# Kernel tuning notes

Hardware: AMD Instinct MI355X
Metric: run time of the kernel (lower is better)

## Reference

```python
import jax, jax.numpy as jnp
import numpy as np

OUT = 7            # output_size
SR = 2             # sampling_ratio (samples per bin per axis)
SCALES = (0.25, 0.125, 0.0625, 0.03125)
CANON_SIZE = 224.0
CANON_LVL = 4.0
MIN_LVL = 2
IMG = 800.0


def setup_inputs() -> dict:
    key = jax.random.key(0)
    kf = jax.random.split(key, 6)
    B, C, R = 2, 256, 256
    sizes = [200, 100, 50, 25]
    feats = [jax.random.normal(kf[i], (B, C, s, s), jnp.float32) for i, s in enumerate(sizes)]
    # valid xyxy boxes in [0, IMG], log-uniform side lengths -> spread across FPN levels
    ctr = jax.random.uniform(kf[4], (B, R, 2), minval=0.0, maxval=IMG)
    wh = jnp.exp(jax.random.uniform(kf[5], (B, R, 2), minval=float(np.log(16.0)), maxval=float(np.log(512.0))))
    lo = jnp.clip(ctr - wh / 2, 0.0, IMG)
    hi = jnp.clip(ctr + wh / 2, 0.0, IMG)
    boxes = jnp.concatenate([lo, hi], axis=-1)  # [B,R,4]
    return {"feat0": feats[0], "feat1": feats[1], "feat2": feats[2], "feat3": feats[3], "boxes": boxes}


def _prep(c, lim):
    """torchvision ROIAlign (aligned=False) bilinear index prep.
    c: sample coords [N,OUT,SR]; lim: per-box feature extent (H or W) [N]."""
    limb = lim[:, None, None]
    valid = (c > -1.0) & (c < limb)          # out-of-range samples contribute 0
    cc = jnp.maximum(c, 0.0)
    low = jnp.floor(cc)
    cap = limb - 1.0
    at_edge = low >= cap                      # y_low >= H-1 -> clamp, frac = 0
    low = jnp.minimum(low, cap)
    high = jnp.minimum(low + 1.0, cap)
    cc = jnp.where(at_edge, low, cc)
    frac = cc - low
    return valid, low.astype(jnp.int32), high.astype(jnp.int32), frac


def roi_pooler(feats, boxes):
    B, R = boxes.shape[0], boxes.shape[1]
    C = feats[0].shape[1]
    N = B * R
    flat = boxes.reshape(N, 4)
    bidx = jnp.repeat(jnp.arange(B, dtype=jnp.int32), R)  # batch index per ROI

    # level assignment (assign_boxes_to_levels)
    area = (flat[:, 2] - flat[:, 0]) * (flat[:, 3] - flat[:, 1])
    lvl = jnp.floor(CANON_LVL + jnp.log2(jnp.sqrt(area) / CANON_SIZE + 1e-8))
    lvl = jnp.clip(lvl, MIN_LVL, MIN_LVL + len(feats) - 1).astype(jnp.int32) - MIN_LVL  # [N] in [0,3]

    # pad all levels to P2 size and stack so each ROI is sampled once at its level
    Hm, Wm = feats[0].shape[2], feats[0].shape[3]
    padded = jnp.stack([jnp.pad(f, ((0, 0), (0, 0), (0, Hm - f.shape[2]), (0, Wm - f.shape[3]))) for f in feats])
    fp = padded.transpose(0, 1, 3, 4, 2)  # [L,B,Hm,Wm,C] channels-last for gather
    Hs = jnp.array([f.shape[2] for f in feats], jnp.float32)[lvl]
    Ws = jnp.array([f.shape[3] for f in feats], jnp.float32)[lvl]
    scale = jnp.array(SCALES, jnp.float32)[lvl]

    # ROIAlign aligned=False: scale coords, clamp roi size to >= 1
    x1 = flat[:, 0] * scale
    y1 = flat[:, 1] * scale
    x2 = flat[:, 2] * scale
    y2 = flat[:, 3] * scale
    roi_w = jnp.maximum(x2 - x1, 1.0)
    roi_h = jnp.maximum(y2 - y1, 1.0)
    bw = roi_w / OUT
    bh = roi_h / OUT

    # sample grid: bin index + sub-sample offsets -> [N,OUT,SR]
    grid = jnp.arange(OUT, dtype=jnp.float32)[None, :, None] + (jnp.arange(SR, dtype=jnp.float32)[None, None, :] + 0.5) / SR
    ys = y1[:, None, None] + bh[:, None, None] * grid
    xs = x1[:, None, None] + bw[:, None, None] * grid

    vy, yl, yh, fy = _prep(ys, Hs)
    vx, xl, xh, fx = _prep(xs, Ws)

    P = OUT * OUT * SR * SR  # all sample points per ROI

    def by(a):  # y-axis quantity -> broadcast over (out_y,out_x,sr_y,sr_x)
        return jnp.broadcast_to(a[:, :, None, :, None], (N, OUT, OUT, SR, SR)).reshape(N, P)

    def bx(a):
        return jnp.broadcast_to(a[:, None, :, None, :], (N, OUT, OUT, SR, SR)).reshape(N, P)

    YL, YH, FY, VY = by(yl), by(yh), by(fy), by(vy)
    XL, XH, FX, VX = bx(xl), bx(xh), bx(fx), bx(vx)

    li = lvl[:, None]
    bi = bidx[:, None]
    v00 = fp[li, bi, YL, XL]  # [N,P,C]
    v01 = fp[li, bi, YL, XH]
    v10 = fp[li, bi, YH, XL]
    v11 = fp[li, bi, YH, XH]

    w = lambda a: a[..., None]
    val = (w((1 - FY) * (1 - FX)) * v00 + w((1 - FY) * FX) * v01
           + w(FY * (1 - FX)) * v10 + w(FY * FX) * v11)
    val = val * w((VY & VX).astype(val.dtype))
    out = val.reshape(N, OUT, OUT, SR * SR, C).mean(axis=3)  # average over SR*SR samples
    return out.transpose(0, 3, 1, 2)  # [N,C,OUT,OUT]


def reference(feat0, feat1, feat2, feat3, boxes):
    return roi_pooler([feat0, feat1, feat2, feat3], boxes)
```

## Files before the change

### kernel.cpp

```cpp
#include <hip/hip_runtime.h>
#include <math.h>

#define OUTSZ 7
#define SRATE 2

#define B_ 2
#define C_ 256
#define R_ 256

__global__ __launch_bounds__(256) void roi_pooler_kernel(
    const float* __restrict__ f0, const float* __restrict__ f1,
    const float* __restrict__ f2, const float* __restrict__ f3,
    const float* __restrict__ boxes, float* __restrict__ out)
{
    const int total = B_ * R_ * C_ * OUTSZ * OUTSZ;
    int idx = blockIdx.x * blockDim.x + threadIdx.x;
    if (idx >= total) return;

    int ox = idx % OUTSZ;
    int oy = (idx / OUTSZ) % OUTSZ;
    int c  = (idx / (OUTSZ * OUTSZ)) % C_;
    int n  = idx / (OUTSZ * OUTSZ * C_);
    int b  = n / R_;

    const float* bx = boxes + (size_t)n * 4;
    float x1 = bx[0], y1 = bx[1], x2 = bx[2], y2 = bx[3];
    float area = (x2 - x1) * (y2 - y1);
    float lf = floorf(4.0f + log2f(sqrtf(area) / 224.0f + 1e-8f));
    lf = fminf(fmaxf(lf, 2.0f), 5.0f);
    int lvl = (int)lf - 2;

    const float scales[4] = {0.25f, 0.125f, 0.0625f, 0.03125f};
    const int   sizes[4]  = {200, 100, 50, 25};
    float scale = scales[lvl];
    int   HW    = sizes[lvl];
    const float* fptr;
    switch (lvl) {
        case 0:  fptr = f0; break;
        case 1:  fptr = f1; break;
        case 2:  fptr = f2; break;
        default: fptr = f3; break;
    }

    float fx1 = x1 * scale, fy1 = y1 * scale;
    float fx2 = x2 * scale, fy2 = y2 * scale;
    float roi_w = fmaxf(fx2 - fx1, 1.0f);
    float roi_h = fmaxf(fy2 - fy1, 1.0f);
    float bw = roi_w / OUTSZ;
    float bh = roi_h / OUTSZ;

    const float* plane = fptr + ((size_t)b * C_ + c) * (size_t)(HW * HW);
    float lim = (float)HW;
    float cap = lim - 1.0f;

    float acc = 0.0f;
    #pragma unroll
    for (int sy = 0; sy < SRATE; sy++) {
        float yc = fy1 + bh * ((float)oy + ((float)sy + 0.5f) / SRATE);
        bool  vy  = (yc > -1.0f) && (yc < lim);
        float ccy = fmaxf(yc, 0.0f);
        float lowy = floorf(ccy);
        bool  ey  = lowy >= cap;
        lowy = fminf(lowy, cap);
        float highy = fminf(lowy + 1.0f, cap);
        float wfy = ey ? 0.0f : (ccy - lowy);
        int yl = (int)lowy, yh = (int)highy;

        #pragma unroll
        for (int sx = 0; sx < SRATE; sx++) {
            float xc = fx1 + bw * ((float)ox + ((float)sx + 0.5f) / SRATE);
            bool  vx  = (xc > -1.0f) && (xc < lim);
            float ccx = fmaxf(xc, 0.0f);
            float lowx = floorf(ccx);
            bool  ex  = lowx >= cap;
            lowx = fminf(lowx, cap);
            float highx = fminf(lowx + 1.0f, cap);
            float wfx = ex ? 0.0f : (ccx - lowx);
            int xl = (int)lowx, xh = (int)highx;

            if (vy && vx) {
                float v00 = plane[yl * HW + xl];
                float v01 = plane[yl * HW + xh];
                float v10 = plane[yh * HW + xl];
                float v11 = plane[yh * HW + xh];
                acc += (1.0f - wfy) * (1.0f - wfx) * v00
                     + (1.0f - wfy) * wfx          * v01
                     + wfy          * (1.0f - wfx) * v10
                     + wfy          * wfx          * v11;
            }
        }
    }

    out[idx] = acc * (1.0f / (SRATE * SRATE));
}

extern "C" void kernel_launch(void* const* d_in, const int* in_sizes, int n_in,
                              void* d_out, int out_size, void* d_ws, size_t ws_size,
                              hipStream_t stream) {
    const float* f0    = (const float*)d_in[0];
    const float* f1    = (const float*)d_in[1];
    const float* f2    = (const float*)d_in[2];
    const float* f3    = (const float*)d_in[3];
    const float* boxes = (const float*)d_in[4];
    float* out = (float*)d_out;

    const int total = B_ * R_ * C_ * OUTSZ * OUTSZ;
    int block = 256;
    int grid = (total + block - 1) / block;
    roi_pooler_kernel<<<grid, block, 0, stream>>>(f0, f1, f2, f3, boxes, out);
}
```

Before: 221.3 us.

## Precompute per-ROI sampling tables and stage ROI patches in shared memory

Adds a prep kernel that computes the level, patch bounds and per-axis bilinear indices and weights for each ROI once, writing them to workspace. The main kernel gives each block one ROI and four channels. It cooperatively loads the ROI's feature patch into LDS with row-contiguous reads, then computes the 49 bins per channel from LDS. Patches too large for LDS fall back to direct global reads. This removes redundant per-thread coordinate math and scattered gathers, at the cost of an extra launch, workspace use, and idle threads (60 of 256) during compute.

```diff
diff --git a/kernel.cpp b/kernel.cpp
--- a/kernel.cpp
+++ b/kernel.cpp
@@ -3,25 +3,24 @@
 
 #define OUTSZ 7
 #define SRATE 2
-
 #define B_ 2
 #define C_ 256
 #define R_ 256
+#define N_ (B_ * R_)
 
-__global__ __launch_bounds__(256) void roi_pooler_kernel(
-    const float* __restrict__ f0, const float* __restrict__ f1,
-    const float* __restrict__ f2, const float* __restrict__ f3,
-    const float* __restrict__ boxes, float* __restrict__ out)
+#define SPAD 1232
+
+struct RoiInfo {
+    int lvl, HW, planeBase0, x0, y0, Wp, Hp, S;
+    float wy0[14], wy1[14], wx0[14], wx1[14];
+    short ylr[14], yhr[14], xlr[14], xhr[14];
+};
+
+__global__ __launch_bounds__(256) void roi_prep(const float* __restrict__ boxes,
+                                                RoiInfo* __restrict__ info)
 {
-    const int total = B_ * R_ * C_ * OUTSZ * OUTSZ;
-    int idx = blockIdx.x * blockDim.x + threadIdx.x;
-    if (idx >= total) return;
-
-    int ox = idx % OUTSZ;
-    int oy = (idx / OUTSZ) % OUTSZ;
-    int c  = (idx / (OUTSZ * OUTSZ)) % C_;
-    int n  = idx / (OUTSZ * OUTSZ * C_);
-    int b  = n / R_;
+    int n = blockIdx.x * 256 + threadIdx.x;
+    if (n >= N_) return;
 
     const float* bx = boxes + (size_t)n * 4;
     float x1 = bx[0], y1 = bx[1], x2 = bx[2], y2 = bx[3];
@@ -34,64 +33,137 @@
     const int   sizes[4]  = {200, 100, 50, 25};
     float scale = scales[lvl];
     int   HW    = sizes[lvl];
-    const float* fptr;
-    switch (lvl) {
-        case 0:  fptr = f0; break;
-        case 1:  fptr = f1; break;
-        case 2:  fptr = f2; break;
-        default: fptr = f3; break;
-    }
 
     float fx1 = x1 * scale, fy1 = y1 * scale;
-    float fx2 = x2 * scale, fy2 = y2 * scale;
-    float roi_w = fmaxf(fx2 - fx1, 1.0f);
-    float roi_h = fmaxf(fy2 - fy1, 1.0f);
-    float bw = roi_w / OUTSZ;
-    float bh = roi_h / OUTSZ;
+    float roi_w = fmaxf(x2 * scale - fx1, 1.0f);
+    float roi_h = fmaxf(y2 * scale - fy1, 1.0f);
+    float bw = roi_w / (float)OUTSZ;
+    float bh = roi_h / (float)OUTSZ;
 
-    const float* plane = fptr + ((size_t)b * C_ + c) * (size_t)(HW * HW);
-    float lim = (float)HW;
-    float cap = lim - 1.0f;
+    int x0 = max(0, (int)floorf(fx1));
+    int y0 = max(0, (int)floorf(fy1));
+    int x1p = min(HW - 1, (int)floorf(fx1 + roi_w) + 1);
+    int y1p = min(HW - 1, (int)floorf(fy1 + roi_h) + 1);
 
-    float acc = 0.0f;
+    RoiInfo ri;
+    ri.lvl = lvl;
+    ri.HW = HW;
+    ri.planeBase0 = (n >> 8) * C_ * HW * HW;
+    ri.x0 = x0; ri.y0 = y0;
+    ri.Wp = x1p - x0 + 1;
+    ri.Hp = y1p - y0 + 1;
+    ri.S = ri.Wp * ri.Hp;
+
+    float lim = (float)HW, cap = lim - 1.0f;
     #pragma unroll
-    for (int sy = 0; sy < SRATE; sy++) {
-        float yc = fy1 + bh * ((float)oy + ((float)sy + 0.5f) / SRATE);
-        bool  vy  = (yc > -1.0f) && (yc < lim);
-        float ccy = fmaxf(yc, 0.0f);
-        float lowy = floorf(ccy);
-        bool  ey  = lowy >= cap;
-        lowy = fminf(lowy, cap);
-        float highy = fminf(lowy + 1.0f, cap);
-        float wfy = ey ? 0.0f : (ccy - lowy);
-        int yl = (int)lowy, yh = (int)highy;
+    for (int i = 0; i < 14; ++i) {
+        float g = (float)(i >> 1) + ((float)(i & 1) + 0.5f) * 0.5f;
+        {
+            float c = fy1 + bh * g;
+            bool  v = (c > -1.0f) && (c < lim);
+            float cc = fmaxf(c, 0.0f);
+            float low = floorf(cc);
+            bool  edge = low >= cap;
+            low = fminf(low, cap);
+            float high = fminf(low + 1.0f, cap);
+            float fr = edge ? 0.0f : (cc - low);
+            ri.ylr[i] = (short)((int)low - y0);
+            ri.yhr[i] = (short)((int)high - y0);
+            ri.wy0[i] = v ? (1.0f - fr) : 0.0f;
+            ri.wy1[i] = v ? fr : 0.0f;
+        }
+        {
+            float c = fx1 + bw * g;
+            bool  v = (c > -1.0f) && (c < lim);
+            float cc = fmaxf(c, 0.0f);
+            float low = floorf(cc);
+            bool  edge = low >= cap;
+            low = fminf(low, cap);
+            float high = fminf(low + 1.0f, cap);
+            float fr = edge ? 0.0f : (cc - low);
+            ri.xlr[i] = (short)((int)low - x0);
+            ri.xhr[i] = (short)((int)high - x0);
+            ri.wx0[i] = v ? (1.0f - fr) : 0.0f;
+            ri.wx1[i] = v ? fr : 0.0f;
+        }
+    }
+    info[n] = ri;
+}
 
+__global__ __launch_bounds__(256) void roi_main(
+    const float* __restrict__ f0, const float* __restrict__ f1,
+    const float* __restrict__ f2, const float* __restrict__ f3,
+    const RoiInfo* __restrict__ info, float* __restrict__ out)
+{
+    const int n = blockIdx.y;
+    const int cbase = blockIdx.x * 4;
+    const int tid = threadIdx.x;
+
+    const RoiInfo& ri = info[n];
+    const int HW = ri.HW, Wp = ri.Wp, Hp = ri.Hp, x0 = ri.x0, y0 = ri.y0, S = ri.S;
+    const float* fl;
+    switch (ri.lvl) {
+        case 0:  fl = f0; break;
+        case 1:  fl = f1; break;
+        case 2:  fl = f2; break;
+        default: fl = f3; break;
+    }
+    const float* base = fl + (size_t)ri.planeBase0;
+    const int planeSz = HW * HW;
+
+    __shared__ float patch[4][SPAD];
+    const bool staged = (S <= SPAD);
+
+    if (staged) {
+        int lw = 32 - __clz(Wp - 1);
+        int xr = tid & ((1 << lw) - 1);
+        int yr0 = tid >> lw;
+        int rpp = 256 >> lw;
         #pragma unroll
-        for (int sx = 0; sx < SRATE; sx++) {
-            float xc = fx1 + bw * ((float)ox + ((float)sx + 0.5f) / SRATE);
-            bool  vx  = (xc > -1.0f) && (xc < lim);
-            float ccx = fmaxf(xc, 0.0f);
-            float lowx = floorf(ccx);
-            bool  ex  = lowx >= cap;
-            lowx = fminf(lowx, cap);
-            float highx = fminf(lowx + 1.0f, cap);
-            float wfx = ex ? 0.0f : (ccx - lowx);
-            int xl = (int)lowx, xh = (int)highx;
-
-            if (vy && vx) {
-                float v00 = plane[yl * HW + xl];
-                float v01 = plane[yl * HW + xh];
-                float v10 = plane[yh * HW + xl];
-                float v11 = plane[yh * HW + xh];
-                acc += (1.0f - wfy) * (1.0f - wfx) * v00
-                     + (1.0f - wfy) * wfx          * v01
-                     + wfy          * (1.0f - wfx) * v10
-                     + wfy          * wfx          * v11;
+        for (int ch = 0; ch < 4; ++ch) {
+            const float* plane = base + (size_t)(cbase + ch) * planeSz;
+            if (xr < Wp) {
+                for (int y = yr0; y < Hp; y += rpp)
+                    patch[ch][y * Wp + xr] = plane[(y0 + y) * HW + x0 + xr];
             }
         }
     }
+    __syncthreads();
 
-    out[idx] = acc * (1.0f / (SRATE * SRATE));
+    if (tid < 196) {
+        int ch = tid / 49;
+        int cell = tid - ch * 49;
+        int oy = cell / 7, ox = cell - oy * 7;
+        const float* plane = base + (size_t)(cbase + ch) * planeSz;
+
+        float acc = 0.0f;
+        #pragma unroll
+        for (int sy = 0; sy < SRATE; ++sy) {
+            int ei = oy * 2 + sy;
+            float wy0 = ri.wy0[ei], wy1 = ri.wy1[ei];
+            int yl = ri.ylr[ei], yh = ri.yhr[ei];
+            #pragma unroll
+            for (int sx = 0; sx < SRATE; ++sx) {
+                int ej = ox * 2 + sx;
+                float wx0 = ri.wx0[ej], wx1 = ri.wx1[ej];
+                int xl = ri.xlr[ej], xh = ri.xhr[ej];
+                float v00, v01, v10, v11;
+                if (staged) {
+                    v00 = patch[ch][yl * Wp + xl];
+                    v01 = patch[ch][yl * Wp + xh];
+                    v10 = patch[ch][yh * Wp + xl];
+                    v11 = patch[ch][yh * Wp + xh];
+                } else {
+                    v00 = plane[(y0 + yl) * HW + x0 + xl];
+                    v01 = plane[(y0 + yl) * HW + x0 + xh];
+                    v10 = plane[(y0 + yh) * HW + x0 + xl];
+                    v11 = plane[(y0 + yh) * HW + x0 + xh];
+                }
+                acc += wy0 * (wx0 * v00 + wx1 * v01) + wy1 * (wx0 * v10 + wx1 * v11);
+            }
+        }
+        out[((size_t)(n * C_ + cbase + ch)) * 49 + cell] = acc * 0.25f;
+    }
 }
 
 extern "C" void kernel_launch(void* const* d_in, const int* in_sizes, int n_in,
@@ -103,9 +175,8 @@
     const float* f3    = (const float*)d_in[3];
     const float* boxes = (const float*)d_in[4];
     float* out = (float*)d_out;
+    RoiInfo* info = (RoiInfo*)d_ws;
 
-    const int total = B_ * R_ * C_ * OUTSZ * OUTSZ;
-    int block = 256;
-    int grid = (total + block - 1) / block;
-    roi_pooler_kernel<<<grid, block, 0, stream>>>(f0, f1, f2, f3, boxes, out);
+    roi_prep<<<dim3((N_ + 255) / 256), 256, 0, stream>>>(boxes, info);
+    roi_main<<<dim3(C_ / 4, N_), 256, 0, stream>>>(f0, f1, f2, f3, info, out);
 }
```

Result: slower. 255.0 us (+15.2%).
